# Performance work log

Measured on AMD Instinct MI355X. Metric: run time of the kernel, lower is better.

Reference implementation:

```python
import jax, jax.numpy as jnp
import numpy as np

B, C, ELL, EQ, E = 1024, 128, 16, 3, 10
P3, P2, P1 = 23, 5, 1


def setup_inputs() -> dict:
    key = jax.random.key(0)
    ks = jax.random.split(key, 8)
    x = jax.random.normal(ks[0], (B, C, ELL), dtype=jnp.float32)
    # element one-hot encoding
    elem = jax.random.randint(ks[1], (B,), 0, E)
    y = jax.nn.one_hot(elem, E, dtype=jnp.float32)
    # U matrices are fixed CG-coefficient tensors (constants); random stand-ins with correct shapes
    U3 = jax.random.normal(ks[2], (EQ, ELL, ELL, ELL, P3), dtype=jnp.float32) * 0.1
    U2 = jax.random.normal(ks[3], (EQ, ELL, ELL, P2), dtype=jnp.float32) * 0.1
    U1 = jax.random.normal(ks[4], (EQ, ELL, P1), dtype=jnp.float32) * 0.1
    # learned per-element weights, init stddev 1/num_params as in the module
    w_max = jax.random.normal(ks[5], (E, P3, C), dtype=jnp.float32) / P3
    w2 = jax.random.normal(ks[6], (E, P2, C), dtype=jnp.float32) / P2
    w1 = jax.random.normal(ks[7], (E, P1, C), dtype=jnp.float32) / P1
    return {"x": x, "y": y, "U3": U3, "U2": U2, "U1": U1,
            "w_max": w_max, "w2": w2, "w1": w1}


def reference(x, y, U3, U2, U1, w_max, w2, w1):
    # per-node element weight gather (y is one-hot over elements)
    wn3 = jnp.einsum('be,ekc->bkc', y, w_max)  # (B, P3, C)
    # main contraction: 'wxvik,ekc,bci,be->bcwxv', ordered to keep intermediates small
    t = jnp.einsum('bkc,bci->bcik', wn3, x)      # (B, C, ELL, P3)
    out = jnp.einsum('wxvik,bcik->bcwxv', U3, t)  # (B, C, EQ, ELL, ELL)
    # nu = 2 step
    wn2 = jnp.einsum('be,ekc->bkc', y, w2)
    c2 = jnp.einsum('wxvk,bkc->bcwxv', U2, wn2) + out
    out = jnp.einsum('bcwxi,bci->bcwx', c2, x)    # (B, C, EQ, ELL)
    # nu = 1 step
    wn1 = jnp.einsum('be,ekc->bkc', y, w1)
    c1 = jnp.einsum('wxk,bkc->bcwx', U1, wn1) + out
    out = jnp.einsum('bcwi,bci->bcw', c1, x)      # (B, C, EQ)
    return out.reshape(out.shape[0], -1)          # (B, C*EQ)
```

## Files before the change

### kernel.cpp

```cpp
#include <hip/hip_runtime.h>

#define B_    1024
#define C_    128
#define ELL   16
#define EQ    3
#define E_    10
#define P3    23
#define P2    5
#define NSEG  176
#define RSTR  180
#define SRS   (48 * RSTR)
#define KD    28

typedef float v2f __attribute__((ext_vector_type(2)));

#define WS_CNT   0
#define WS_LIST  64
#define WS_S     65536

#define SEG_OFF_INIT {0,20,36,52,68,84,96,108,120,132,140,148,156,164,168,172}

__device__ void do_lists(const float* __restrict__ y, int* __restrict__ cnt_g,
                         int* __restrict__ list_g, int t) {
    __shared__ int lcnt[E_];
    if (t < E_) lcnt[t] = 0;
    __syncthreads();
    for (int r = 0; r < 4; ++r) {
        int b = t + 256 * r;
        int e = 0;
        #pragma unroll
        for (int j = 1; j < E_; ++j)
            if (y[b * E_ + j] > 0.5f) e = j;
        int slot = atomicAdd(&lcnt[e], 1);
        list_g[e * B_ + slot] = b;
    }
    __syncthreads();
    if (t < E_) {
        int c0 = lcnt[t];
        cnt_g[t] = c0;
        int last = (c0 > 0) ? list_g[t * B_ + c0 - 1] : 0;
        int cp = (c0 + 63) & ~63;
        if (cp > B_) cp = B_;
        for (int s2 = c0; s2 < cp; ++s2) list_g[t * B_ + s2] = last;
    }
}

__global__ __launch_bounds__(256, 2) void k_s(const float* __restrict__ U3,
                                              const float* __restrict__ U2,
                                              const float* __restrict__ wmax,
                                              const float* __restrict__ w2,
                                              const float* __restrict__ y,
                                              float* __restrict__ Sg,
                                              int* __restrict__ cnt_g,
                                              int* __restrict__ list_g) {
    const int t = threadIdx.x;
    if (blockIdx.x == 48) {
        if (blockIdx.y == 0 && blockIdx.z == 0) do_lists(y, cnt_g, list_g, t);
        return;
    }
    __shared__ __align__(16) float wsm[KD * 32];
    __shared__ __align__(16) float SKL[NSEG * KD];

    const int j  = blockIdx.x;
    const int e  = blockIdx.y;
    const int cq = blockIdx.z;

    for (int idx = t; idx < KD * 32; idx += 256) {
        int k = idx >> 5, cc = idx & 31, c = cq * 32 + cc;
        wsm[idx] = (k < 23) ? wmax[(e * P3 + k) * C_ + c]
                            : w2[(e * P2 + (k - 23)) * C_ + c];
    }

    if (t < NSEG) {
        const int SO[16] = SEG_OFF_INIT;
        int v = 0;
        #pragma unroll
        for (int s = 1; s < 16; ++s) v += (t >= SO[s]) ? 1 : 0;
        const int l    = t - SO[v];
        const int real = 17 - v;

        float row[KD];
        #pragma unroll
        for (int d = 0; d < KD; ++d) row[d] = 0.f;

        if (l == 0) {
            #pragma unroll
            for (int q = 0; q < P2; ++q)
                row[23 + q] = U2[(size_t)j * (ELL * P2) + v * P2 + q];
        } else if (l < real) {
            int i = v + l - 1;
            const float* pa = U3 + (size_t)j * (ELL * ELL * P3) + (v * ELL + i) * P3;
            const float* pb = U3 + (size_t)j * (ELL * ELL * P3) + (i * ELL + v) * P3;
            if (i != v) {
                #pragma unroll
                for (int k = 0; k < P3; ++k) row[k] = pa[k] + pb[k];
            } else {
                #pragma unroll
                for (int k = 0; k < P3; ++k) row[k] = pa[k];
            }
        }

        float* dst = &SKL[t * KD];
        #pragma unroll
        for (int d4 = 0; d4 < KD / 4; ++d4)
            *(float4*)(dst + 4 * d4) = make_float4(row[4 * d4], row[4 * d4 + 1],
                                                   row[4 * d4 + 2], row[4 * d4 + 3]);
    }
    __syncthreads();

    if (t >= NSEG) return;

    const int sg = t % 44;
    const int cg = t / 44;
    const int c8 = cg * 8;

    v2f acc[4][4];
    #pragma unroll
    for (int s = 0; s < 4; ++s)
        #pragma unroll
        for (int cp2 = 0; cp2 < 4; ++cp2) acc[s][cp2] = (v2f){0.f, 0.f};

    #pragma unroll
    for (int k4 = 0; k4 < KD / 4; ++k4) {
        float4 sk4[4];
        #pragma unroll
        for (int s = 0; s < 4; ++s)
            sk4[s] = *(const float4*)&SKL[(sg + 44 * s) * KD + 4 * k4];
        #pragma unroll
        for (int kk = 0; kk < 4; ++kk) {
            const int k = 4 * k4 + kk;
            float4 w0 = *(const float4*)&wsm[k * 32 + c8];
            float4 w1 = *(const float4*)&wsm[k * 32 + c8 + 4];
            v2f wp0 = {w0.x, w0.y}, wp1 = {w0.z, w0.w};
            v2f wp2 = {w1.x, w1.y}, wp3 = {w1.z, w1.w};
            #pragma unroll
            for (int s = 0; s < 4; ++s) {
                const float skv = (kk == 0) ? sk4[s].x : (kk == 1) ? sk4[s].y
                                : (kk == 2) ? sk4[s].z : sk4[s].w;
                acc[s][0] += skv * wp0;
                acc[s][1] += skv * wp1;
                acc[s][2] += skv * wp2;
                acc[s][3] += skv * wp3;
            }
        }
    }

    #pragma unroll
    for (int s = 0; s < 4; ++s) {
        const int slot = sg + 44 * s;
        #pragma unroll
        for (int cc = 0; cc < 8; ++cc) {
            const int c = cq * 32 + c8 + cc;
            Sg[(size_t)(e * C_ + c) * SRS + j * RSTR + slot] = acc[s][cc >> 1][cc & 1];
        }
    }
}

__global__ __launch_bounds__(256, 2) void k_main(
    const float* __restrict__ x, const float* __restrict__ Sg,
    const float* __restrict__ U1, const float* __restrict__ w1,
    const int* __restrict__ cnt_g, const int* __restrict__ list_g,
    float* __restrict__ out) {

    __shared__ __align__(16) float V3L[16 * RSTR];

    const int t  = threadIdx.x;
    const int bx = blockIdx.x;
    const int w  = bx % 3, c = bx / 3;
    const int e  = blockIdx.y;
    const int xx = t & 15, bs = t >> 4;
    const int cnt  = cnt_g[e];
    const int cntp = (cnt + 63) & ~63;

    {
        const float4* src = (const float4*)(Sg + (size_t)(e * C_ + c) * SRS
                                            + (size_t)w * 16 * RSTR);
        float4* dst = (float4*)V3L;
        #pragma unroll
        for (int r = 0; r < 2; ++r) dst[t + 256 * r] = src[t + 256 * r];
        if (t < 208) dst[512 + t] = src[512 + t];
    }
    const float v1x = U1[w * 16 + xx] * w1[e * C_ + c];
    __syncthreads();

    const float* v3p = &V3L[xx * RSTR];
    const int SO[16] = SEG_OFF_INIT;

    #pragma clang loop unroll(disable)
    for (int base = 0; base < cntp; base += 64) {
        __syncthreads();

        const int slot = base + bs * 4;
        int bidx[4];
        #pragma unroll
        for (int r = 0; r < 4; ++r) bidx[r] = list_g[e * B_ + slot + r];

        v2f xm2[2][16];
        float xo[4];
        #pragma unroll
        for (int r = 0; r < 4; ++r) {
            const float* xb = x + ((size_t)bidx[r] * C_ + c) * ELL;
            #pragma unroll
            for (int i4 = 0; i4 < 4; ++i4) {
                float4 a = ((const float4*)xb)[i4];
                xm2[r >> 1][4 * i4 + 0][r & 1] = a.x;
                xm2[r >> 1][4 * i4 + 1][r & 1] = a.y;
                xm2[r >> 1][4 * i4 + 2][r & 1] = a.z;
                xm2[r >> 1][4 * i4 + 3][r & 1] = a.w;
            }
            xo[r] = xb[xx];
        }

        v2f t2p[2] = {(v2f){0.f, 0.f}, (v2f){0.f, 0.f}};
        #pragma unroll
        for (int v = 0; v < 16; ++v) {
            const int off = SO[v];
            const int nf4 = (v == 0) ? 5 : (v < 5) ? 4 : (v < 9) ? 3 : (v < 13) ? 2 : 1;
            v2f inner[2];
            {
                float4 u = *(const float4*)(v3p + off);
                #pragma unroll
                for (int p = 0; p < 2; ++p) {
                    v2f s = u.x + u.y * xm2[p][v];
                    if (v + 1 <= 15) s += u.z * xm2[p][v + 1];
                    if (v + 2 <= 15) s += u.w * xm2[p][v + 2];
                    inner[p] = s;
                }
            }
            #pragma unroll
            for (int q = 1; q < nf4; ++q) {
                float4 u = *(const float4*)(v3p + off + 4 * q);
                const int i0 = v + 4 * q - 1;
                #pragma unroll
                for (int p = 0; p < 2; ++p) {
                    inner[p] += u.x * xm2[p][i0];
                    if (i0 + 1 <= 15) inner[p] += u.y * xm2[p][i0 + 1];
                    if (i0 + 2 <= 15) inner[p] += u.z * xm2[p][i0 + 2];
                    if (i0 + 3 <= 15) inner[p] += u.w * xm2[p][i0 + 3];
                }
            }
            #pragma unroll
            for (int p = 0; p < 2; ++p) t2p[p] += xm2[p][v] * inner[p];
        }

        float cv[4];
        cv[0] = (t2p[0][0] + v1x) * xo[0];
        cv[1] = (t2p[0][1] + v1x) * xo[1];
        cv[2] = (t2p[1][0] + v1x) * xo[2];
        cv[3] = (t2p[1][1] + v1x) * xo[3];
        #pragma unroll
        for (int m = 1; m < 16; m <<= 1) {
            #pragma unroll
            for (int r = 0; r < 4; ++r) cv[r] += __shfl_xor(cv[r], m, 16);
        }
        if (xx == 0) {
            #pragma unroll
            for (int r = 0; r < 4; ++r)
                if (slot + r < cnt)
                    out[(size_t)bidx[r] * (C_ * EQ) + c * EQ + w] = cv[r];
        }
    }
}

extern "C" void kernel_launch(void* const* d_in, const int* in_sizes, int n_in,
                              void* d_out, int out_size, void* d_ws, size_t ws_size,
                              hipStream_t stream) {
    const float* x    = (const float*)d_in[0];
    const float* y    = (const float*)d_in[1];
    const float* U3   = (const float*)d_in[2];
    const float* U2   = (const float*)d_in[3];
    const float* U1   = (const float*)d_in[4];
    const float* wmax = (const float*)d_in[5];
    const float* w2   = (const float*)d_in[6];
    const float* w1   = (const float*)d_in[7];
    float* out = (float*)d_out;
    char*  ws  = (char*)d_ws;

    int*   cnt_g  = (int*)(ws + WS_CNT);
    int*   list_g = (int*)(ws + WS_LIST);
    float* Sg     = (float*)(ws + WS_S);
    (void)ws_size;

    k_s<<<dim3(49, E_, 4), 256, 0, stream>>>(U3, U2, wmax, w2, y, Sg, cnt_g, list_g);
    k_main<<<dim3(C_ * EQ, E_), 256, 0, stream>>>(x, Sg, U1, w1, cnt_g, list_g, out);
}
```

Measured before the change: 124.2 us.

## Map one batch item per thread in k_main, reading S coefficients from global

Restructures k_main so each of 128 threads handles one batch item and loops over all 16 x rows itself. This removes the shared-memory staging of the V3 coefficient block, the per-iteration barriers and the 16-lane shuffle reduction. All threads of a block read the same S addresses, which are wave-uniform, so they can be served as broadcast or scalar loads from cache. List padding moves to multiples of 128 to match. The trade-off is 16x more arithmetic per thread with fewer threads per block, which risks more register pressure and lower parallelism.

```diff
diff --git a/kernel.cpp b/kernel.cpp
--- a/kernel.cpp
+++ b/kernel.cpp
@@ -39,7 +39,7 @@
         int c0 = lcnt[t];
         cnt_g[t] = c0;
         int last = (c0 > 0) ? list_g[t * B_ + c0 - 1] : 0;
-        int cp = (c0 + 63) & ~63;
+        int cp = (c0 + 127) & ~127;
         if (cp > B_) cp = B_;
         for (int s2 = c0; s2 < cp; ++s2) list_g[t * B_ + s2] = last;
     }
@@ -156,109 +156,67 @@
     }
 }
 
-__global__ __launch_bounds__(256, 2) void k_main(
+__global__ __launch_bounds__(128, 4) void k_main(
     const float* __restrict__ x, const float* __restrict__ Sg,
     const float* __restrict__ U1, const float* __restrict__ w1,
     const int* __restrict__ cnt_g, const int* __restrict__ list_g,
     float* __restrict__ out) {
 
-    __shared__ __align__(16) float V3L[16 * RSTR];
-
     const int t  = threadIdx.x;
     const int bx = blockIdx.x;
     const int w  = bx % 3, c = bx / 3;
     const int e  = blockIdx.y;
-    const int xx = t & 15, bs = t >> 4;
     const int cnt  = cnt_g[e];
-    const int cntp = (cnt + 63) & ~63;
-
-    {
-        const float4* src = (const float4*)(Sg + (size_t)(e * C_ + c) * SRS
-                                            + (size_t)w * 16 * RSTR);
-        float4* dst = (float4*)V3L;
-        #pragma unroll
-        for (int r = 0; r < 2; ++r) dst[t + 256 * r] = src[t + 256 * r];
-        if (t < 208) dst[512 + t] = src[512 + t];
-    }
-    const float v1x = U1[w * 16 + xx] * w1[e * C_ + c];
-    __syncthreads();
-
-    const float* v3p = &V3L[xx * RSTR];
+    const int cntp = (cnt + 127) & ~127;
+
+    const float w1ec = w1[e * C_ + c];
+    const float* sbase = Sg + (size_t)(e * C_ + c) * SRS + (size_t)w * 16 * RSTR;
     const int SO[16] = SEG_OFF_INIT;
 
     #pragma clang loop unroll(disable)
-    for (int base = 0; base < cntp; base += 64) {
-        __syncthreads();
-
-        const int slot = base + bs * 4;
-        int bidx[4];
-        #pragma unroll
-        for (int r = 0; r < 4; ++r) bidx[r] = list_g[e * B_ + slot + r];
-
-        v2f xm2[2][16];
-        float xo[4];
-        #pragma unroll
-        for (int r = 0; r < 4; ++r) {
-            const float* xb = x + ((size_t)bidx[r] * C_ + c) * ELL;
+    for (int bb = t; bb < cntp; bb += 128) {
+        const int b = list_g[e * B_ + bb];
+        const float* xb = x + ((size_t)b * C_ + c) * ELL;
+
+        float xm[16];
+        #pragma unroll
+        for (int i4 = 0; i4 < 4; ++i4) {
+            float4 a = ((const float4*)xb)[i4];
+            xm[4 * i4 + 0] = a.x; xm[4 * i4 + 1] = a.y;
+            xm[4 * i4 + 2] = a.z; xm[4 * i4 + 3] = a.w;
+        }
+
+        float oacc = 0.f;
+        #pragma unroll
+        for (int xx = 0; xx < 16; ++xx) {
+            const float* srow = sbase + xx * RSTR;
+            float t2 = 0.f;
             #pragma unroll
-            for (int i4 = 0; i4 < 4; ++i4) {
-                float4 a = ((const float4*)xb)[i4];
-                xm2[r >> 1][4 * i4 + 0][r & 1] = a.x;
-                xm2[r >> 1][4 * i4 + 1][r & 1] = a.y;
-                xm2[r >> 1][4 * i4 + 2][r & 1] = a.z;
-                xm2[r >> 1][4 * i4 + 3][r & 1] = a.w;
+            for (int v = 0; v < 16; ++v) {
+                const int off = SO[v];
+                const int nf4 = (v == 0) ? 5 : (v < 5) ? 4 : (v < 9) ? 3
+                              : (v < 13) ? 2 : 1;
+                float4 u = *(const float4*)(srow + off);
+                float s = u.x + u.y * xm[v];
+                if (v + 1 <= 15) s += u.z * xm[v + 1];
+                if (v + 2 <= 15) s += u.w * xm[v + 2];
+                #pragma unroll
+                for (int q = 1; q < nf4; ++q) {
+                    float4 u2 = *(const float4*)(srow + off + 4 * q);
+                    const int i0 = v + 4 * q - 1;
+                    s += u2.x * xm[i0];
+                    if (i0 + 1 <= 15) s += u2.y * xm[i0 + 1];
+                    if (i0 + 2 <= 15) s += u2.z * xm[i0 + 2];
+                    if (i0 + 3 <= 15) s += u2.w * xm[i0 + 3];
+                }
+                t2 += xm[v] * s;
             }
-            xo[r] = xb[xx];
-        }
-
-        v2f t2p[2] = {(v2f){0.f, 0.f}, (v2f){0.f, 0.f}};
-        #pragma unroll
-        for (int v = 0; v < 16; ++v) {
-            const int off = SO[v];
-            const int nf4 = (v == 0) ? 5 : (v < 5) ? 4 : (v < 9) ? 3 : (v < 13) ? 2 : 1;
-            v2f inner[2];
-            {
-                float4 u = *(const float4*)(v3p + off);
-                #pragma unroll
-                for (int p = 0; p < 2; ++p) {
-                    v2f s = u.x + u.y * xm2[p][v];
-                    if (v + 1 <= 15) s += u.z * xm2[p][v + 1];
-                    if (v + 2 <= 15) s += u.w * xm2[p][v + 2];
-                    inner[p] = s;
-                }
-            }
-            #pragma unroll
-            for (int q = 1; q < nf4; ++q) {
-                float4 u = *(const float4*)(v3p + off + 4 * q);
-                const int i0 = v + 4 * q - 1;
-                #pragma unroll
-                for (int p = 0; p < 2; ++p) {
-                    inner[p] += u.x * xm2[p][i0];
-                    if (i0 + 1 <= 15) inner[p] += u.y * xm2[p][i0 + 1];
-                    if (i0 + 2 <= 15) inner[p] += u.z * xm2[p][i0 + 2];
-                    if (i0 + 3 <= 15) inner[p] += u.w * xm2[p][i0 + 3];
-                }
-            }
-            #pragma unroll
-            for (int p = 0; p < 2; ++p) t2p[p] += xm2[p][v] * inner[p];
-        }
-
-        float cv[4];
-        cv[0] = (t2p[0][0] + v1x) * xo[0];
-        cv[1] = (t2p[0][1] + v1x) * xo[1];
-        cv[2] = (t2p[1][0] + v1x) * xo[2];
-        cv[3] = (t2p[1][1] + v1x) * xo[3];
-        #pragma unroll
-        for (int m = 1; m < 16; m <<= 1) {
-            #pragma unroll
-            for (int r = 0; r < 4; ++r) cv[r] += __shfl_xor(cv[r], m, 16);
-        }
-        if (xx == 0) {
-            #pragma unroll
-            for (int r = 0; r < 4; ++r)
-                if (slot + r < cnt)
-                    out[(size_t)bidx[r] * (C_ * EQ) + c * EQ + w] = cv[r];
-        }
+            const float v1x = U1[w * 16 + xx] * w1ec;
+            oacc += (t2 + v1x) * xm[xx];
+        }
+
+        if (bb < cnt)
+            out[(size_t)b * (C_ * EQ) + c * EQ + w] = oacc;
     }
 }
 
@@ -282,5 +240,5 @@
     (void)ws_size;
 
     k_s<<<dim3(49, E_, 4), 256, 0, stream>>>(U3, U2, wmax, w2, y, Sg, cnt_g, list_g);
-    k_main<<<dim3(C_ * EQ, E_), 256, 0, stream>>>(x, Sg, U1, w1, cnt_g, list_g, out);
-}
+    k_main<<<dim3(C_ * EQ, E_), 128, 0, stream>>>(x, Sg, U1, w1, cnt_g, list_g, out);
+}
```

Measured after the change: 200.6 us. 1.62x slower.
